# Kernel optimization log

Measured on AMD Instinct MI355X. Metric: run time of the kernel, lower is better.

The kernel has to match this reference:

```python
import jax, jax.numpy as jnp
import numpy as np

BS, QS, H, NH, HD = 2, 2048, 1024, 16, 64


def setup_inputs() -> dict:
    key = jax.random.key(0)
    ks = jax.random.split(key, 10)
    s = 0.02
    x = jax.random.normal(ks[0], (BS, QS, H), jnp.float32)
    pos_emb = jax.random.normal(ks[1], (QS, H), jnp.float32)
    rr_bias = jax.random.normal(ks[2], (NH, HD), jnp.float32) * s
    rw_bias = jax.random.normal(ks[3], (NH, HD), jnp.float32) * s
    Wq = jax.random.normal(ks[4], (H, NH * HD), jnp.float32) * s
    Wk = jax.random.normal(ks[5], (H, NH * HD), jnp.float32) * s
    Wv = jax.random.normal(ks[6], (H, NH * HD), jnp.float32) * s
    Wr = jax.random.normal(ks[7], (H, NH * HD), jnp.float32) * s
    Wo = jax.random.normal(ks[8], (NH * HD, H), jnp.float32) * s
    ln_gamma = jnp.ones((H,), jnp.float32)
    ln_beta = jnp.zeros((H,), jnp.float32)
    # True = masked (filled with -inf); strict causal mask, ms = ks - qs = 0
    mask = jnp.triu(jnp.ones((QS, QS), bool), 1)
    return {"x": x, "mask": mask, "pos_emb": pos_emb, "rr_bias": rr_bias,
            "rw_bias": rw_bias, "Wq": Wq, "Wk": Wk, "Wv": Wv, "Wr": Wr,
            "Wo": Wo, "ln_gamma": ln_gamma, "ln_beta": ln_beta}


def _left_shift(x, bs):
    # x: [bs, qs, ks, n_head] -- Transformer-XL relative-shift trick
    b, qs, ksz, nh = x.shape
    pad = jnp.zeros((b, qs, 1, nh), x.dtype)
    xp = jnp.concatenate([pad, x], axis=2).reshape(b, ksz + 1, qs, nh)
    x = xp[:, 1:].reshape(b, qs, ksz, nh)
    # NOTE: original code uses diagonal offset (ks - bs) with bs = batch size
    tri = jnp.tril(jnp.ones((qs, ksz), x.dtype), ksz - bs)
    return x * tri[None, :, :, None]


def reference(x, mask, pos_emb, rr_bias, rw_bias, Wq, Wk, Wv, Wr, Wo, ln_gamma, ln_beta):
    bs, qs, hid = x.shape
    nh, dh = rr_bias.shape
    ksz = qs  # self-attention, no memory
    scale = 1.0 / dh ** 0.5
    q = (x @ Wq).reshape(bs, qs, nh, dh)
    k = (x @ Wk).reshape(bs, ksz, nh, dh)
    v = (x @ Wv).reshape(bs, ksz, nh, dh)
    r = (pos_emb @ Wr).reshape(qs, nh, dh)
    AC = jnp.einsum('bqnd,bknd->bqkn', q + rw_bias[None, None], k)
    BD = jnp.einsum('bqnd,knd->bqkn', q + rr_bias[None, None], r)
    BD = _left_shift(BD, bs)
    score = (AC + BD) * scale
    score = jnp.where(mask[None, :, :, None], -jnp.inf, score)
    prob = jax.nn.softmax(score, axis=2)  # softmax over key axis
    att = jnp.einsum('bqkn,bknd->bqnd', prob, v)
    out = att.reshape(bs, qs, nh * dh) @ Wo
    out = x + out  # residual (post-lnorm variant)
    mu = out.mean(-1, keepdims=True)
    var = ((out - mu) ** 2).mean(-1, keepdims=True)
    return (out - mu) / jnp.sqrt(var + 1e-5) * ln_gamma + ln_beta
```

## Files before the change

kernel.cpp:

```cpp
#include <hip/hip_runtime.h>
#include <hip/hip_bf16.h>


typedef _Float16 f16;
typedef __attribute__((ext_vector_type(8))) _Float16 f16x8;
typedef __attribute__((ext_vector_type(4))) float f32x4;

__global__ __launch_bounds__(256) void cast_kernel(const float* __restrict__ in,
                                                   f16* __restrict__ out, int n4) {
  int i = blockIdx.x * 256 + threadIdx.x;
  if (i >= n4) return;
  f32x4 v = *(const f32x4*)&in[i * 4];
  f16 o0 = (f16)v[0], o1 = (f16)v[1], o2 = (f16)v[2], o3 = (f16)v[3];
  f16* p = &out[i * 4];
  p[0] = o0; p[1] = o1; p[2] = o2; p[3] = o3;
}

__global__ __launch_bounds__(256) void wtrans_kernel(const float* __restrict__ W,
                                                     f16* __restrict__ WT) {
  __shared__ float tile[32][33];
  int k0 = blockIdx.x * 32, n0 = blockIdx.y * 32;
  int tx = threadIdx.x, ty = threadIdx.y;
#pragma unroll
  for (int i = 0; i < 4; ++i)
    tile[ty + i * 8][tx] = W[(size_t)(k0 + ty + i * 8) * 1024 + n0 + tx];
  __syncthreads();
#pragma unroll
  for (int i = 0; i < 4; ++i)
    WT[(size_t)(n0 + ty + i * 8) * 1024 + k0 + tx] = (f16)tile[tx][ty + i * 8];
}

__global__ __launch_bounds__(256) void gemm_qkv(
    const f16* __restrict__ A, const f16* __restrict__ Bq, const f16* __restrict__ Bk,
    const f16* __restrict__ Bv, f16* __restrict__ Qw, f16* __restrict__ Qr,
    f16* __restrict__ Kb, f16* __restrict__ VTb,
    const float* __restrict__ rw, const float* __restrict__ rr) {
  constexpr int LD = 72;
  __shared__ f16 sm[2 * 128 * LD];
  f16* As = sm;
  f16* Bs = sm + 128 * LD;
  const int bsel = blockIdx.x >> 3;
  const f16* Bw = bsel == 0 ? Bq : (bsel == 1 ? Bk : Bv);
  const int n0 = (blockIdx.x & 7) * 128, m0 = blockIdx.y * 128;
  const int tid = threadIdx.x, lane = tid & 63, wv = tid >> 6;
  const int wm = wv >> 1, wn = wv & 1, lg = lane >> 4, ln = lane & 15;
  f32x4 acc[4][4] = {};
  const int srow = tid >> 1, scb = (tid & 1) * 32;
  const f16* ga = A + (size_t)(m0 + srow) * 1024 + scb;
  const f16* gb = Bw + (size_t)(n0 + srow) * 1024 + scb;
  f16* as_w = &As[srow * LD + scb];
  f16* bs_w = &Bs[srow * LD + scb];

  for (int kt = 0; kt < 16; ++kt) {
    __syncthreads();
#pragma unroll
    for (int i = 0; i < 4; ++i) {
      *(f16x8*)&as_w[i * 8] = *(const f16x8*)&ga[kt * 64 + i * 8];
      *(f16x8*)&bs_w[i * 8] = *(const f16x8*)&gb[kt * 64 + i * 8];
    }
    __syncthreads();
#pragma unroll
    for (int ks = 0; ks < 2; ++ks) {
      f16x8 af[4], bfr[4];
#pragma unroll
      for (int mi = 0; mi < 4; ++mi)
        af[mi] = *(const f16x8*)&As[(wm * 64 + mi * 16 + ln) * LD + ks * 32 + 8 * lg];
#pragma unroll
      for (int ni = 0; ni < 4; ++ni)
        bfr[ni] = *(const f16x8*)&Bs[(wn * 64 + ni * 16 + ln) * LD + ks * 32 + 8 * lg];
#pragma unroll
      for (int mi = 0; mi < 4; ++mi)
#pragma unroll
        for (int ni = 0; ni < 4; ++ni)
          acc[mi][ni] = __builtin_amdgcn_mfma_f32_16x16x32_f16(af[mi], bfr[ni],
                                                               acc[mi][ni], 0, 0, 0);
    }
  }

  if (bsel == 2) {
    __syncthreads();
    f16* T = sm;
#pragma unroll
    for (int mi = 0; mi < 4; ++mi)
#pragma unroll
      for (int ni = 0; ni < 4; ++ni)
#pragma unroll
        for (int r = 0; r < 4; ++r) {
          int ml = wm * 64 + mi * 16 + 4 * lg + r;
          int cl = wn * 64 + ni * 16 + ln;
          T[cl * 136 + ml] = (f16)acc[mi][ni][r];
        }
    __syncthreads();
    int cl = tid >> 1, mb = (tid & 1) * 64;
    int gc = n0 + cl, gm = m0 + mb;
    int hh = gc >> 6, dd = gc & 63, bb = gm >> 11, ss = gm & 2047;
    f16* dst = VTb + ((size_t)(bb * 16 + hh) * 64 + dd) * 2048 + ss;
    const f16* srcT = &T[cl * 136 + mb];
#pragma unroll
    for (int i = 0; i < 8; ++i) *(f16x8*)&dst[i * 8] = *(const f16x8*)&srcT[i * 8];
  } else {
#pragma unroll
    for (int mi = 0; mi < 4; ++mi)
#pragma unroll
      for (int ni = 0; ni < 4; ++ni)
#pragma unroll
        for (int r = 0; r < 4; ++r) {
          int m = m0 + wm * 64 + mi * 16 + 4 * lg + r;
          int c = n0 + wn * 64 + ni * 16 + ln;
          float v = acc[mi][ni][r];
          size_t off = (size_t)m * 1024 + c;
          if (bsel == 0) {
            Qw[off] = (f16)(v + rw[c]);
            Qr[off] = (f16)(v + rr[c]);
          } else {
            Kb[off] = (f16)v;
          }
        }
  }
}

template <int MODE>
__global__ __launch_bounds__(256) void gemm64(
    const f16* __restrict__ A, const f16* __restrict__ Bw,
    f16* __restrict__ out0, float* __restrict__ fout, const float* __restrict__ xres) {
  constexpr int LD = 72;
  __shared__ f16 As[64 * LD];
  __shared__ f16 Bs[128 * LD];
  const int tid = threadIdx.x, lane = tid & 63, wv = tid >> 6;
  const int wm = wv >> 1, wn = wv & 1, lg = lane >> 4, ln = lane & 15;
  const int m0 = blockIdx.y * 64, n0 = blockIdx.x * 128;
  f32x4 acc[2][4] = {};
  const int ra = tid >> 2, ca = (tid & 3) * 16;
  const int rb = tid >> 1, cb = (tid & 1) * 32;
  const f16* ga = A + (size_t)(m0 + ra) * 1024 + ca;
  const f16* gb = Bw + (size_t)(n0 + rb) * 1024 + cb;
  f16* as_w = &As[ra * LD + ca];
  f16* bs_w = &Bs[rb * LD + cb];

  for (int kt = 0; kt < 16; ++kt) {
    __syncthreads();
#pragma unroll
    for (int i = 0; i < 2; ++i)
      *(f16x8*)&as_w[i * 8] = *(const f16x8*)&ga[kt * 64 + i * 8];
#pragma unroll
    for (int i = 0; i < 4; ++i)
      *(f16x8*)&bs_w[i * 8] = *(const f16x8*)&gb[kt * 64 + i * 8];
    __syncthreads();
#pragma unroll
    for (int ks = 0; ks < 2; ++ks) {
      f16x8 af[2], bfr[4];
#pragma unroll
      for (int mi = 0; mi < 2; ++mi)
        af[mi] = *(const f16x8*)&As[(wm * 32 + mi * 16 + ln) * LD + ks * 32 + 8 * lg];
#pragma unroll
      for (int ni = 0; ni < 4; ++ni)
        bfr[ni] = *(const f16x8*)&Bs[(wn * 64 + ni * 16 + ln) * LD + ks * 32 + 8 * lg];
#pragma unroll
      for (int mi = 0; mi < 2; ++mi)
#pragma unroll
        for (int ni = 0; ni < 4; ++ni)
          acc[mi][ni] = __builtin_amdgcn_mfma_f32_16x16x32_f16(af[mi], bfr[ni],
                                                               acc[mi][ni], 0, 0, 0);
    }
  }
#pragma unroll
  for (int mi = 0; mi < 2; ++mi)
#pragma unroll
    for (int ni = 0; ni < 4; ++ni)
#pragma unroll
      for (int r = 0; r < 4; ++r) {
        int m = m0 + wm * 32 + mi * 16 + 4 * lg + r;
        int c = n0 + wn * 64 + ni * 16 + ln;
        size_t off = (size_t)m * 1024 + c;
        if (MODE == 3) out0[off] = (f16)acc[mi][ni][r];
        else fout[off] = acc[mi][ni][r] + xres[off];
      }
}

__device__ __forceinline__ void chunk_map(int c, int& qt, int& ci) {
  if (c < 8) { qt = c; ci = 0; }
  else if (c < 24) { qt = 8 + ((c - 8) >> 1); ci = (c - 8) & 1; }
  else if (c < 48) { int d = c - 24; qt = 16 + d / 3; ci = d % 3; }
  else { int d = c - 48; qt = 24 + (d >> 2); ci = d & 3; }
}

__global__ __launch_bounds__(256) void attn_chunk(
    const f16* __restrict__ Qw, const f16* __restrict__ Qr,
    const f16* __restrict__ Kb, const f16* __restrict__ VT,
    const f16* __restrict__ Rb, f16* __restrict__ attb,
    f16* __restrict__ Opart, float* __restrict__ Mlp) {
  constexpr int LD = 72;
  constexpr int MW = 88;
  __shared__ f16 Kl[64 * LD];
  __shared__ f16 Vl[64 * LD];
  __shared__ f16 Rl[128 * LD];
  __shared__ f16 Sl[64 * MW];

  int qt, ci;
  chunk_map(blockIdx.x, qt, ci);
  const int h = blockIdx.y, b = blockIdx.z;
  const int q0 = qt * 64;
  const int kts = ci * 8;
  const int kte = min(kts + 7, qt);
  const int tid = threadIdx.x, lane = tid & 63, wv = tid >> 6;
  const int lg = lane >> 4, ln = lane & 15;

  const size_t qoff = ((size_t)(b * 2048 + q0 + wv * 16 + ln) * 16 + h) * 64 + 8 * lg;
  f16x8 aqw[2], aqr[2];
  aqw[0] = *(const f16x8*)&Qw[qoff];
  aqw[1] = *(const f16x8*)&Qw[qoff + 32];
  aqr[0] = *(const f16x8*)&Qr[qoff];
  aqr[1] = *(const f16x8*)&Qr[qoff + 32];

  f32x4 oacc[4] = {};
  float mrun[4] = {-1e30f, -1e30f, -1e30f, -1e30f};
  float lrun[4] = {0.f, 0.f, 0.f, 0.f};

  const int r4 = tid >> 2, c16 = (tid & 3) * 16;
  const int r2 = tid >> 1, c32 = (tid & 1) * 32;
  const int t0 = 48 - 16 * wv;

  f16x8 pk[2], pv[2], pr[4];
  auto load_regs = [&](int kt) {
    const int k0 = kt * 64;
    const f16* ksrc = Kb + ((size_t)(b * 2048 + k0 + r4) * 16 + h) * 64 + c16;
    pk[0] = *(const f16x8*)&ksrc[0];
    pk[1] = *(const f16x8*)&ksrc[8];
    const f16* vsrc = VT + ((size_t)(b * 16 + h) * 64 + r4) * 2048 + k0 + c16;
    pv[0] = *(const f16x8*)&vsrc[0];
    pv[1] = *(const f16x8*)&vsrc[8];
    const int j = 1984 - q0 + k0 + r2;
    if (j < 2048) {
      const f16* rsrc = Rb + ((size_t)j * 16 + h) * 64 + c32;
#pragma unroll
      for (int i = 0; i < 4; ++i) pr[i] = *(const f16x8*)&rsrc[i * 8];
    } else {
      f16x8 z = {};
#pragma unroll
      for (int i = 0; i < 4; ++i) pr[i] = z;
    }
  };
  auto write_lds = [&]() {
    *(f16x8*)&Kl[r4 * LD + c16] = pk[0];
    *(f16x8*)&Kl[r4 * LD + c16 + 8] = pk[1];
    *(f16x8*)&Vl[r4 * LD + c16] = pv[0];
    *(f16x8*)&Vl[r4 * LD + c16 + 8] = pv[1];
#pragma unroll
    for (int i = 0; i < 4; ++i) *(f16x8*)&Rl[r2 * LD + c32 + i * 8] = pr[i];
  };

  load_regs(kts);
  write_lds();
  __syncthreads();

  for (int kt = kts; kt <= kte; ++kt) {
    const int k0 = kt * 64;
    if (kt < kte) load_regs(kt + 1);

    f32x4 sc[4] = {};
#pragma unroll
    for (int ks = 0; ks < 2; ++ks)
#pragma unroll
      for (int ni = 0; ni < 4; ++ni) {
        f16x8 kf = *(const f16x8*)&Kl[(ni * 16 + ln) * LD + ks * 32 + 8 * lg];
        sc[ni] = __builtin_amdgcn_mfma_f32_16x16x32_f16(aqw[ks], kf, sc[ni], 0, 0, 0);
      }

    f32x4 mw[5] = {};
#pragma unroll
    for (int ks = 0; ks < 2; ++ks)
#pragma unroll
      for (int nj = 0; nj < 5; ++nj) {
        f16x8 rf = *(const f16x8*)&Rl[(t0 + nj * 16 + ln) * LD + ks * 32 + 8 * lg];
        mw[nj] = __builtin_amdgcn_mfma_f32_16x16x32_f16(aqr[ks], rf, mw[nj], 0, 0, 0);
      }

#pragma unroll
    for (int nj = 0; nj < 5; ++nj)
#pragma unroll
      for (int r = 0; r < 4; ++r)
        Sl[(wv * 16 + 4 * lg + r) * MW + nj * 16 + ln] = (f16)mw[nj][r];

#pragma unroll
    for (int ni = 0; ni < 4; ++ni)
#pragma unroll
      for (int r = 0; r < 4; ++r) {
        int ql = 4 * lg + r;
        int ki = ni * 16 + ln;
        float bd = (float)Sl[(wv * 16 + ql) * MW + ki - ql + 15];
        float s = (sc[ni][r] + bd) * 0.125f;
        if (k0 + ki > q0 + wv * 16 + ql) s = -1e30f;
        sc[ni][r] = s;
      }

#pragma unroll
    for (int r = 0; r < 4; ++r) {
      float mx = sc[0][r];
#pragma unroll
      for (int ni = 1; ni < 4; ++ni) mx = fmaxf(mx, sc[ni][r]);
#pragma unroll
      for (int off = 1; off < 16; off <<= 1) mx = fmaxf(mx, __shfl_xor(mx, off, 16));
      float mnew = fmaxf(mrun[r], mx);
      float corr = __expf(mrun[r] - mnew);
      mrun[r] = mnew;
      float rs = 0.f;
#pragma unroll
      for (int ni = 0; ni < 4; ++ni) {
        float p = __expf(sc[ni][r] - mnew);
        sc[ni][r] = p;
        rs += p;
      }
#pragma unroll
      for (int off = 1; off < 16; off <<= 1) rs += __shfl_xor(rs, off, 16);
      lrun[r] = lrun[r] * corr + rs;
#pragma unroll
      for (int ni = 0; ni < 4; ++ni) oacc[ni][r] *= corr;
    }

#pragma unroll
    for (int ni = 0; ni < 4; ++ni)
#pragma unroll
      for (int r = 0; r < 4; ++r)
        Sl[(wv * 16 + 4 * lg + r) * MW + ni * 16 + ln] = (f16)sc[ni][r];

#pragma unroll
    for (int ks = 0; ks < 2; ++ks) {
      f16x8 pf = *(const f16x8*)&Sl[(wv * 16 + ln) * MW + ks * 32 + 8 * lg];
#pragma unroll
      for (int ni = 0; ni < 4; ++ni) {
        f16x8 vf = *(const f16x8*)&Vl[(ni * 16 + ln) * LD + ks * 32 + 8 * lg];
        oacc[ni] = __builtin_amdgcn_mfma_f32_16x16x32_f16(pf, vf, oacc[ni], 0, 0, 0);
      }
    }

    __syncthreads();
    if (kt < kte) {
      write_lds();
      __syncthreads();
    }
  }

  if (qt < 8) {
#pragma unroll
    for (int ni = 0; ni < 4; ++ni)
#pragma unroll
      for (int r = 0; r < 4; ++r)
        Sl[(wv * 16 + 4 * lg + r) * MW + ni * 16 + ln] = (f16)(oacc[ni][r] / lrun[r]);
#pragma unroll
    for (int i = 0; i < 2; ++i) {
      int row = wv * 16 + i * 8 + (lane >> 3);
      int col = (lane & 7) * 8;
      *(f16x8*)&attb[((size_t)(b * 2048 + q0 + row) * 16 + h) * 64 + col] =
          *(const f16x8*)&Sl[row * MW + col];
    }
  } else {
    const size_t pidx = (size_t)(b * 16 + h) * 80 + blockIdx.x;
#pragma unroll
    for (int ni = 0; ni < 4; ++ni)
#pragma unroll
      for (int r = 0; r < 4; ++r)
        Sl[(wv * 16 + 4 * lg + r) * MW + ni * 16 + ln] = (f16)oacc[ni][r];
    if (ln == 0) {
#pragma unroll
      for (int r = 0; r < 4; ++r) {
        int row = wv * 16 + 4 * lg + r;
        Mlp[pidx * 128 + row] = mrun[r];
        Mlp[pidx * 128 + 64 + row] = lrun[r];
      }
    }
#pragma unroll
    for (int i = 0; i < 2; ++i) {
      int row = wv * 16 + i * 8 + (lane >> 3);
      int col = (lane & 7) * 8;
      *(f16x8*)&Opart[pidx * 4096 + row * 64 + col] = *(const f16x8*)&Sl[row * MW + col];
    }
  }
}

__global__ __launch_bounds__(256) void combine_kernel(
    const f16* __restrict__ Opart, const float* __restrict__ Mlp,
    f16* __restrict__ attb) {
  const int qt = 8 + blockIdx.x, h = blockIdx.y, b = blockIdx.z;
  const int nc = (qt + 8) >> 3;
  int cbase;
  if (qt < 16) cbase = 8 + 2 * (qt - 8);
  else if (qt < 24) cbase = 24 + 3 * (qt - 16);
  else cbase = 48 + 4 * (qt - 24);
  const int tid = threadIdx.x;
  const int row = tid >> 2, d0 = (tid & 3) * 16;
  const size_t pbase = (size_t)(b * 16 + h) * 80 + cbase;

  float m[4], l[4], w[4];
  float M = -1e30f;
#pragma unroll
  for (int i = 0; i < 4; ++i)
    if (i < nc) {
      m[i] = Mlp[(pbase + i) * 128 + row];
      l[i] = Mlp[(pbase + i) * 128 + 64 + row];
      M = fmaxf(M, m[i]);
    }
  float wsum = 0.f;
#pragma unroll
  for (int i = 0; i < 4; ++i)
    if (i < nc) {
      w[i] = __expf(m[i] - M);
      wsum += w[i] * l[i];
    }
  float o[16] = {};
#pragma unroll
  for (int i = 0; i < 4; ++i)
    if (i < nc) {
      const f16* src = &Opart[(pbase + i) * 4096 + row * 64 + d0];
      f16x8 v0 = *(const f16x8*)&src[0];
      f16x8 v1 = *(const f16x8*)&src[8];
#pragma unroll
      for (int j = 0; j < 8; ++j) {
        o[j] += w[i] * (float)v0[j];
        o[8 + j] += w[i] * (float)v1[j];
      }
    }
  float inv = 1.f / wsum;
  f16x8 r0, r1;
#pragma unroll
  for (int j = 0; j < 8; ++j) {
    r0[j] = (f16)(o[j] * inv);
    r1[j] = (f16)(o[8 + j] * inv);
  }
  f16* dst = &attb[((size_t)(b * 2048 + qt * 64 + row) * 16 + h) * 64 + d0];
  *(f16x8*)&dst[0] = r0;
  *(f16x8*)&dst[8] = r1;
}

__global__ __launch_bounds__(256) void ln_kernel(const float* __restrict__ pre,
                                                 const float* __restrict__ gamma,
                                                 const float* __restrict__ beta,
                                                 float* __restrict__ out) {
  __shared__ float red[8];
  const int row = blockIdx.x, t = threadIdx.x;
  f32x4 v = *(const f32x4*)&pre[(size_t)row * 1024 + t * 4];
  float s = v[0] + v[1] + v[2] + v[3];
  float s2 = v[0] * v[0] + v[1] * v[1] + v[2] * v[2] + v[3] * v[3];
#pragma unroll
  for (int off = 1; off < 64; off <<= 1) {
    s += __shfl_xor(s, off, 64);
    s2 += __shfl_xor(s2, off, 64);
  }
  if ((t & 63) == 0) {
    red[t >> 6] = s;
    red[(t >> 6) + 4] = s2;
  }
  __syncthreads();
  s = red[0] + red[1] + red[2] + red[3];
  s2 = red[4] + red[5] + red[6] + red[7];
  float mean = s * (1.f / 1024.f);
  float var = s2 * (1.f / 1024.f) - mean * mean;
  float rcp = rsqrtf(var + 1e-5f);
  f32x4 g = *(const f32x4*)&gamma[t * 4];
  f32x4 be = *(const f32x4*)&beta[t * 4];
  f32x4 o;
#pragma unroll
  for (int j = 0; j < 4; ++j) o[j] = (v[j] - mean) * rcp * g[j] + be[j];
  *(f32x4*)&out[(size_t)row * 1024 + t * 4] = o;
}

extern "C" void kernel_launch(void* const* d_in, const int* in_sizes, int n_in,
                              void* d_out, int out_size, void* d_ws, size_t ws_size,
                              hipStream_t stream) {
  const float* x = (const float*)d_in[0];
  const float* pe = (const float*)d_in[2];
  const float* rr = (const float*)d_in[3];
  const float* rw = (const float*)d_in[4];
  const float* Wq = (const float*)d_in[5];
  const float* Wk = (const float*)d_in[6];
  const float* Wv = (const float*)d_in[7];
  const float* Wr = (const float*)d_in[8];
  const float* Wo = (const float*)d_in[9];
  const float* gamma = (const float*)d_in[10];
  const float* beta = (const float*)d_in[11];
  float* out = (float*)d_out;

  char* w = (char*)d_ws;
  auto alloc = [&](size_t bytes) {
    char* p = w;
    w += (bytes + 255) & ~(size_t)255;
    return p;
  };
  float* preln = (float*)alloc(4096ull * 1024 * 4);
  f16* xb = (f16*)alloc(4096ull * 1024 * 2);
  f16* pb = (f16*)alloc(2048ull * 1024 * 2);
  f16* WTq = (f16*)alloc(1024ull * 1024 * 2);
  f16* WTk = (f16*)alloc(1024ull * 1024 * 2);
  f16* WTv = (f16*)alloc(1024ull * 1024 * 2);
  f16* WTr = (f16*)alloc(1024ull * 1024 * 2);
  f16* WTo = (f16*)alloc(1024ull * 1024 * 2);
  f16* Qw = (f16*)alloc(4096ull * 1024 * 2);
  f16* Qr = (f16*)alloc(4096ull * 1024 * 2);
  f16* Kb = (f16*)alloc(4096ull * 1024 * 2);
  f16* VTb = (f16*)alloc(4096ull * 1024 * 2);
  f16* Rb = (f16*)alloc(2048ull * 1024 * 2);
  f16* attb = (f16*)alloc(4096ull * 1024 * 2);
  f16* Opart = (f16*)alloc(2ull * 16 * 80 * 4096 * 2);
  float* Mlp = (float*)alloc(2ull * 16 * 80 * 128 * 4);

  cast_kernel<<<4096, 256, 0, stream>>>(x, xb, 4096 * 1024 / 4);
  cast_kernel<<<2048, 256, 0, stream>>>(pe, pb, 2048 * 1024 / 4);
  dim3 tb(32, 8);
  wtrans_kernel<<<dim3(32, 32), tb, 0, stream>>>(Wq, WTq);
  wtrans_kernel<<<dim3(32, 32), tb, 0, stream>>>(Wk, WTk);
  wtrans_kernel<<<dim3(32, 32), tb, 0, stream>>>(Wv, WTv);
  wtrans_kernel<<<dim3(32, 32), tb, 0, stream>>>(Wr, WTr);
  wtrans_kernel<<<dim3(32, 32), tb, 0, stream>>>(Wo, WTo);

  gemm_qkv<<<dim3(24, 32), 256, 0, stream>>>(xb, WTq, WTk, WTv, Qw, Qr, Kb, VTb, rw, rr);
  gemm64<3><<<dim3(8, 32), 256, 0, stream>>>(pb, WTr, Rb, nullptr, nullptr);

  attn_chunk<<<dim3(80, 16, 2), 256, 0, stream>>>(Qw, Qr, Kb, VTb, Rb, attb, Opart, Mlp);
  combine_kernel<<<dim3(24, 16, 2), 256, 0, stream>>>(Opart, Mlp, attb);

  gemm64<4><<<dim3(8, 64), 256, 0, stream>>>(attb, WTo, nullptr, preln, x);
  ln_kernel<<<4096, 256, 0, stream>>>(preln, gamma, beta, out);
}
```

Measured before the change: 343.4 us.

## Use direct-to-LDS loads in GEMMs, shuffle-based rel-shift, and fuse prep launches

GEMM tile loads now use global_load_lds to move data straight from global memory into LDS with an unpadded 64-wide layout, which avoids staging through registers. In attention, the relative-shift of the BD scores uses cross-lane shuffles instead of writing to shared memory and reading back. The cast and weight-transpose launches are merged into single kernels to cut launch overhead. The unpadded LDS layout may introduce bank conflicts on the fragment reads.

```diff
diff --git a/kernel.cpp b/kernel.cpp
--- a/kernel.cpp
+++ b/kernel.cpp
@@ -6,19 +6,42 @@
 typedef __attribute__((ext_vector_type(8))) _Float16 f16x8;
 typedef __attribute__((ext_vector_type(4))) float f32x4;
 
-__global__ __launch_bounds__(256) void cast_kernel(const float* __restrict__ in,
-                                                   f16* __restrict__ out, int n4) {
+__device__ __forceinline__ void gload16(const f16* g, f16* l) {
+  __builtin_amdgcn_global_load_lds((__attribute__((address_space(1))) void*)(g),
+                                   (__attribute__((address_space(3))) void*)(l), 16, 0, 0);
+}
+
+__global__ __launch_bounds__(256) void cast2_kernel(const float* __restrict__ a,
+                                                    f16* __restrict__ ao, int na4,
+                                                    const float* __restrict__ b,
+                                                    f16* __restrict__ bo, int nb4) {
   int i = blockIdx.x * 256 + threadIdx.x;
-  if (i >= n4) return;
-  f32x4 v = *(const f32x4*)&in[i * 4];
+  const float* src;
+  f16* dst;
+  int j;
+  if (i < na4) { src = a; dst = ao; j = i; }
+  else { j = i - na4; if (j >= nb4) return; src = b; dst = bo; }
+  f32x4 v = *(const f32x4*)&src[j * 4];
   f16 o0 = (f16)v[0], o1 = (f16)v[1], o2 = (f16)v[2], o3 = (f16)v[3];
-  f16* p = &out[i * 4];
+  f16* p = &dst[j * 4];
   p[0] = o0; p[1] = o1; p[2] = o2; p[3] = o3;
 }
 
-__global__ __launch_bounds__(256) void wtrans_kernel(const float* __restrict__ W,
-                                                     f16* __restrict__ WT) {
+__global__ __launch_bounds__(256) void wtrans5_kernel(
+    const float* __restrict__ W0, const float* __restrict__ W1, const float* __restrict__ W2,
+    const float* __restrict__ W3, const float* __restrict__ W4,
+    f16* __restrict__ T0, f16* __restrict__ T1, f16* __restrict__ T2,
+    f16* __restrict__ T3, f16* __restrict__ T4) {
   __shared__ float tile[32][33];
+  const float* W;
+  f16* WT;
+  switch (blockIdx.z) {
+    case 0: W = W0; WT = T0; break;
+    case 1: W = W1; WT = T1; break;
+    case 2: W = W2; WT = T2; break;
+    case 3: W = W3; WT = T3; break;
+    default: W = W4; WT = T4; break;
+  }
   int k0 = blockIdx.x * 32, n0 = blockIdx.y * 32;
   int tx = threadIdx.x, ty = threadIdx.y;
 #pragma unroll
@@ -35,28 +58,24 @@
     const f16* __restrict__ Bv, f16* __restrict__ Qw, f16* __restrict__ Qr,
     f16* __restrict__ Kb, f16* __restrict__ VTb,
     const float* __restrict__ rw, const float* __restrict__ rr) {
-  constexpr int LD = 72;
-  __shared__ f16 sm[2 * 128 * LD];
+  __shared__ f16 sm[17408];
   f16* As = sm;
-  f16* Bs = sm + 128 * LD;
+  f16* Bs = sm + 8192;
   const int bsel = blockIdx.x >> 3;
   const f16* Bw = bsel == 0 ? Bq : (bsel == 1 ? Bk : Bv);
   const int n0 = (blockIdx.x & 7) * 128, m0 = blockIdx.y * 128;
   const int tid = threadIdx.x, lane = tid & 63, wv = tid >> 6;
   const int wm = wv >> 1, wn = wv & 1, lg = lane >> 4, ln = lane & 15;
+  const int srow = lane >> 3, scol = (lane & 7) * 8;
   f32x4 acc[4][4] = {};
-  const int srow = tid >> 1, scb = (tid & 1) * 32;
-  const f16* ga = A + (size_t)(m0 + srow) * 1024 + scb;
-  const f16* gb = Bw + (size_t)(n0 + srow) * 1024 + scb;
-  f16* as_w = &As[srow * LD + scb];
-  f16* bs_w = &Bs[srow * LD + scb];
 
   for (int kt = 0; kt < 16; ++kt) {
     __syncthreads();
 #pragma unroll
     for (int i = 0; i < 4; ++i) {
-      *(f16x8*)&as_w[i * 8] = *(const f16x8*)&ga[kt * 64 + i * 8];
-      *(f16x8*)&bs_w[i * 8] = *(const f16x8*)&gb[kt * 64 + i * 8];
+      int c = wv * 4 + i;
+      gload16(A + (size_t)(m0 + c * 8 + srow) * 1024 + kt * 64 + scol, &As[c * 512]);
+      gload16(Bw + (size_t)(n0 + c * 8 + srow) * 1024 + kt * 64 + scol, &Bs[c * 512]);
     }
     __syncthreads();
 #pragma unroll
@@ -64,10 +83,10 @@
       f16x8 af[4], bfr[4];
 #pragma unroll
       for (int mi = 0; mi < 4; ++mi)
-        af[mi] = *(const f16x8*)&As[(wm * 64 + mi * 16 + ln) * LD + ks * 32 + 8 * lg];
+        af[mi] = *(const f16x8*)&As[(wm * 64 + mi * 16 + ln) * 64 + ks * 32 + 8 * lg];
 #pragma unroll
       for (int ni = 0; ni < 4; ++ni)
-        bfr[ni] = *(const f16x8*)&Bs[(wn * 64 + ni * 16 + ln) * LD + ks * 32 + 8 * lg];
+        bfr[ni] = *(const f16x8*)&Bs[(wn * 64 + ni * 16 + ln) * 64 + ks * 32 + 8 * lg];
 #pragma unroll
       for (int mi = 0; mi < 4; ++mi)
 #pragma unroll
@@ -123,38 +142,36 @@
 __global__ __launch_bounds__(256) void gemm64(
     const f16* __restrict__ A, const f16* __restrict__ Bw,
     f16* __restrict__ out0, float* __restrict__ fout, const float* __restrict__ xres) {
-  constexpr int LD = 72;
-  __shared__ f16 As[64 * LD];
-  __shared__ f16 Bs[128 * LD];
+  __shared__ f16 As[4096];
+  __shared__ f16 Bs[8192];
   const int tid = threadIdx.x, lane = tid & 63, wv = tid >> 6;
   const int wm = wv >> 1, wn = wv & 1, lg = lane >> 4, ln = lane & 15;
   const int m0 = blockIdx.y * 64, n0 = blockIdx.x * 128;
+  const int srow = lane >> 3, scol = (lane & 7) * 8;
   f32x4 acc[2][4] = {};
-  const int ra = tid >> 2, ca = (tid & 3) * 16;
-  const int rb = tid >> 1, cb = (tid & 1) * 32;
-  const f16* ga = A + (size_t)(m0 + ra) * 1024 + ca;
-  const f16* gb = Bw + (size_t)(n0 + rb) * 1024 + cb;
-  f16* as_w = &As[ra * LD + ca];
-  f16* bs_w = &Bs[rb * LD + cb];
 
   for (int kt = 0; kt < 16; ++kt) {
     __syncthreads();
 #pragma unroll
-    for (int i = 0; i < 2; ++i)
-      *(f16x8*)&as_w[i * 8] = *(const f16x8*)&ga[kt * 64 + i * 8];
-#pragma unroll
-    for (int i = 0; i < 4; ++i)
-      *(f16x8*)&bs_w[i * 8] = *(const f16x8*)&gb[kt * 64 + i * 8];
+    for (int i = 0; i < 2; ++i) {
+      int c = wv * 2 + i;
+      gload16(A + (size_t)(m0 + c * 8 + srow) * 1024 + kt * 64 + scol, &As[c * 512]);
+    }
+#pragma unroll
+    for (int i = 0; i < 4; ++i) {
+      int c = wv * 4 + i;
+      gload16(Bw + (size_t)(n0 + c * 8 + srow) * 1024 + kt * 64 + scol, &Bs[c * 512]);
+    }
     __syncthreads();
 #pragma unroll
     for (int ks = 0; ks < 2; ++ks) {
       f16x8 af[2], bfr[4];
 #pragma unroll
       for (int mi = 0; mi < 2; ++mi)
-        af[mi] = *(const f16x8*)&As[(wm * 32 + mi * 16 + ln) * LD + ks * 32 + 8 * lg];
+        af[mi] = *(const f16x8*)&As[(wm * 32 + mi * 16 + ln) * 64 + ks * 32 + 8 * lg];
 #pragma unroll
       for (int ni = 0; ni < 4; ++ni)
-        bfr[ni] = *(const f16x8*)&Bs[(wn * 64 + ni * 16 + ln) * LD + ks * 32 + 8 * lg];
+        bfr[ni] = *(const f16x8*)&Bs[(wn * 64 + ni * 16 + ln) * 64 + ks * 32 + 8 * lg];
 #pragma unroll
       for (int mi = 0; mi < 2; ++mi)
 #pragma unroll
@@ -190,7 +207,7 @@
     const f16* __restrict__ Rb, f16* __restrict__ attb,
     f16* __restrict__ Opart, float* __restrict__ Mlp) {
   constexpr int LD = 72;
-  constexpr int MW = 88;
+  constexpr int MW = 72;
   __shared__ f16 Kl[64 * LD];
   __shared__ f16 Vl[64 * LD];
   __shared__ f16 Rl[128 * LD];
@@ -276,21 +293,18 @@
       }
 
 #pragma unroll
-    for (int nj = 0; nj < 5; ++nj)
-#pragma unroll
-      for (int r = 0; r < 4; ++r)
-        Sl[(wv * 16 + 4 * lg + r) * MW + nj * 16 + ln] = (f16)mw[nj][r];
-
-#pragma unroll
     for (int ni = 0; ni < 4; ++ni)
 #pragma unroll
       for (int r = 0; r < 4; ++r) {
-        int ql = 4 * lg + r;
-        int ki = ni * 16 + ln;
-        float bd = (float)Sl[(wv * 16 + ql) * MW + ki - ql + 15];
-        float s = (sc[ni][r] + bd) * 0.125f;
-        if (k0 + ki > q0 + wv * 16 + ql) s = -1e30f;
-        sc[ni][r] = s;
+        const int s = 15 - 4 * lg - r;
+        const int src = (ln + s) & 15;
+        float v0 = __shfl(mw[ni][r], src, 16);
+        float v1 = __shfl(mw[ni + 1][r], src, 16);
+        float bd = (ln + s < 16) ? v0 : v1;
+        float sv = (sc[ni][r] + bd) * 0.125f;
+        int ql = 4 * lg + r, ki = ni * 16 + ln;
+        if (k0 + ki > q0 + wv * 16 + ql) sv = -1e30f;
+        sc[ni][r] = sv;
       }
 
 #pragma unroll
@@ -502,14 +516,9 @@
   f16* Opart = (f16*)alloc(2ull * 16 * 80 * 4096 * 2);
   float* Mlp = (float*)alloc(2ull * 16 * 80 * 128 * 4);
 
-  cast_kernel<<<4096, 256, 0, stream>>>(x, xb, 4096 * 1024 / 4);
-  cast_kernel<<<2048, 256, 0, stream>>>(pe, pb, 2048 * 1024 / 4);
-  dim3 tb(32, 8);
-  wtrans_kernel<<<dim3(32, 32), tb, 0, stream>>>(Wq, WTq);
-  wtrans_kernel<<<dim3(32, 32), tb, 0, stream>>>(Wk, WTk);
-  wtrans_kernel<<<dim3(32, 32), tb, 0, stream>>>(Wv, WTv);
-  wtrans_kernel<<<dim3(32, 32), tb, 0, stream>>>(Wr, WTr);
-  wtrans_kernel<<<dim3(32, 32), tb, 0, stream>>>(Wo, WTo);
+  cast2_kernel<<<6144, 256, 0, stream>>>(x, xb, 4096 * 1024 / 4, pe, pb, 2048 * 1024 / 4);
+  wtrans5_kernel<<<dim3(32, 32, 5), dim3(32, 8), 0, stream>>>(Wq, Wk, Wv, Wr, Wo,
+                                                              WTq, WTk, WTv, WTr, WTo);
 
   gemm_qkv<<<dim3(24, 32), 256, 0, stream>>>(xb, WTq, WTk, WTv, Qw, Qr, Kb, VTb, rw, rr);
   gemm64<3><<<dim3(8, 32), 256, 0, stream>>>(pb, WTr, Rb, nullptr, nullptr);
```

Measured after the change: 348.3 us. About the same (+1.4%).
